# Kernel optimization log

Measured on AMD Instinct MI355X. Metric: run time of the kernel, lower is better.

Reference implementation:

```python
import jax, jax.numpy as jnp
import numpy as np
import math

B, LA, LB, D, H = 8, 2048, 2048, 512, 512

def setup_inputs() -> dict:
    key = jax.random.key(0)
    ks = jax.random.split(key, 6)
    return {
        "input_a": jax.random.normal(ks[0], (B, LA, D), dtype=jnp.float32),
        "input_b": jax.random.normal(ks[1], (B, LB, D), dtype=jnp.float32),
        "mask_a": jax.random.randint(ks[2], (B, LA), 0, 2, dtype=jnp.int32),
        "mask_b": jax.random.randint(ks[3], (B, LB), 0, 2, dtype=jnp.int32),
        "Wa": jax.random.normal(ks[4], (D, H), dtype=jnp.float32) * (1.0 / math.sqrt(D)),
        "ba": jnp.zeros((H,), dtype=jnp.float32),
        "Wb": jax.random.normal(ks[5], (D, H), dtype=jnp.float32) * (1.0 / math.sqrt(D)),
        "bb": jnp.zeros((H,), dtype=jnp.float32),
    }

def reference(input_a, input_b, mask_a, mask_b, Wa, ba, Wb, bb):
    scale = 1.0 / math.sqrt(D)  # math.sqrt(input_dim_a)
    mapped_a = input_a @ Wa + ba            # [B, La, H]
    mapped_b = input_b @ Wb + bb            # [B, Lb, H]
    # final_mask = (mask_a outer mask_b) == 0
    final_mask = (mask_a[:, :, None] * mask_b[:, None, :]) == 0  # [B, La, Lb]
    scores = jnp.einsum('bih,bjh->bij', mapped_a, mapped_b) * scale
    scores = jnp.where(final_mask, jnp.float32(-1e9), scores)
    # attentions_a = softmax over Lb; attentions_b^T = softmax over La axis
    att_a = jax.nn.softmax(scores, axis=-1)   # [B, La, Lb]
    att_bT = jax.nn.softmax(scores, axis=1)   # [B, La, Lb] (= attentions_b.transpose(1,2))
    output_a = jnp.einsum('bij,bjd->bid', att_bT, input_b)  # [B, La, D]
    output_b = jnp.einsum('bij,bid->bjd', att_a, input_a)   # [B, Lb, D]
    return (output_a + input_a, output_b + input_b)
```

## Files before the change

### kernel.cpp

```cpp
#include <hip/hip_runtime.h>
#include <hip/hip_bf16.h>

#define BATCH 8
#define LSEQ 2048
#define DDIM 512

using f32x4 = __attribute__((ext_vector_type(4))) float;
using s16x8 = __attribute__((ext_vector_type(8))) short;

static __device__ __forceinline__ unsigned short f2b(float f) {
  __hip_bfloat16 h = __float2bfloat16(f);
  return __builtin_bit_cast(unsigned short, h);
}
static __device__ __forceinline__ float b2f(unsigned short u) {
  unsigned int v = ((unsigned int)u) << 16;
  return __builtin_bit_cast(float, v);
}

static __device__ __forceinline__ void gld16(const unsigned short* g, unsigned short* l) {
  __builtin_amdgcn_global_load_lds(
      (__attribute__((address_space(1))) void*)(g),
      (__attribute__((address_space(3))) void*)(l), 16, 0, 0);
}

__device__ __forceinline__ void mfma_kloop2(
    const unsigned short* __restrict__ A, const unsigned short* __restrict__ Bt,
    int K, int lda, int ldb, unsigned short* sA, unsigned short* sB,
    int tid, f32x4 acc[4][4]) {
  const int wave = tid >> 6, lane = tid & 63;
  const int wm = (wave >> 1) * 64, wn = (wave & 1) * 64;
  const int lr = lane & 15, lq = lane >> 4;
  const int srow = tid >> 2;
  const int sk = (tid & 3) * 8;
  unsigned short* dA0 = sA + wave * 512;
  unsigned short* dA1 = sA + 2048 + wave * 512;
  unsigned short* dB0 = sB + wave * 512;
  unsigned short* dB1 = sB + 2048 + wave * 512;
  const unsigned short* pa0 = A + (size_t)srow * lda + sk;
  const unsigned short* pa1 = A + (size_t)(srow + 64) * lda + sk;
  const unsigned short* pb0 = Bt + (size_t)srow * ldb + sk;
  const unsigned short* pb1 = Bt + (size_t)(srow + 64) * ldb + sk;
  gld16(pa0, dA0);
  gld16(pa1, dA1);
  gld16(pb0, dB0);
  gld16(pb1, dB1);
  asm volatile("s_waitcnt vmcnt(0)" ::: "memory");
  __builtin_amdgcn_s_barrier();
  int cur = 0;
  for (int k0 = 0; k0 < K; k0 += 32) {
    const int nxt = cur ^ 1;
    if (k0 + 32 < K) {
      const int off = nxt * 4096;
      gld16(pa0 + k0 + 32, dA0 + off);
      gld16(pa1 + k0 + 32, dA1 + off);
      gld16(pb0 + k0 + 32, dB0 + off);
      gld16(pb1 + k0 + 32, dB1 + off);
    }
    const unsigned short* cA = sA + cur * 4096;
    const unsigned short* cB = sB + cur * 4096;
    s16x8 af[4], bf[4];
#pragma unroll
    for (int r = 0; r < 4; ++r)
      af[r] = *(const s16x8*)(cA + (wm + r * 16 + lr) * 32 + lq * 8);
#pragma unroll
    for (int c = 0; c < 4; ++c)
      bf[c] = *(const s16x8*)(cB + (wn + c * 16 + lr) * 32 + lq * 8);
#pragma unroll
    for (int r = 0; r < 4; ++r)
#pragma unroll
      for (int c = 0; c < 4; ++c)
        acc[r][c] = __builtin_amdgcn_mfma_f32_16x16x32_bf16(af[r], bf[c], acc[r][c], 0, 0, 0);
    asm volatile("s_waitcnt vmcnt(0)" ::: "memory");
    __builtin_amdgcn_s_barrier();
    cur = nxt;
  }
}

__global__ __launch_bounds__(256) void k_prep(const float* __restrict__ in_a,
                                              const float* __restrict__ in_b,
                                              const int* __restrict__ ma,
                                              const int* __restrict__ mb,
                                              unsigned short* __restrict__ oa,
                                              unsigned short* __restrict__ ob,
                                              float* __restrict__ Pa,
                                              float* __restrict__ Pb) {
  int z = blockIdx.z;
  const float* in = z ? in_b : in_a;
  const int* mask = z ? mb : ma;
  unsigned short* o16 = z ? ob : oa;
  float* partial = z ? Pb : Pa;
  int b = blockIdx.y;
  int l0 = blockIdx.x * 32;
  __shared__ int sm[32];
  if (threadIdx.x < 32) sm[threadIdx.x] = mask[b * LSEQ + l0 + threadIdx.x];
  __syncthreads();
  int d = threadIdx.x * 2;
  const float* base = in + ((size_t)b * LSEQ + l0) * DDIM + d;
  unsigned short* obase = o16 + ((size_t)b * LSEQ + l0) * DDIM + d;
  float ax = 0.f, ay = 0.f;
#pragma unroll 4
  for (int r = 0; r < 32; ++r) {
    float2 v = *(const float2*)(base + (size_t)r * DDIM);
    ushort2 u; u.x = f2b(v.x); u.y = f2b(v.y);
    *(ushort2*)(obase + (size_t)r * DDIM) = u;
    if (sm[r] == 0) { ax += v.x; ay += v.y; }
  }
  float2 o; o.x = ax; o.y = ay;
  *(float2*)(partial + ((size_t)(b * 64 + blockIdx.x)) * DDIM + d) = o;
}

__global__ __launch_bounds__(256) void k_p2(const float* __restrict__ Pa,
                                            const float* __restrict__ Pb,
                                            float* __restrict__ Ca,
                                            float* __restrict__ Cb) {
  int g = blockIdx.x;
  const float* src = (g < 8) ? Pa : Pb;
  float* dst = (g < 8) ? Ca : Cb;
  int b = g & 7;
  int d = threadIdx.x * 2;
  float ax = 0.f, ay = 0.f;
  for (int c = 0; c < 64; ++c) {
    float2 v = *(const float2*)(src + ((size_t)(b * 64 + c)) * DDIM + d);
    ax += v.x; ay += v.y;
  }
  dst[b * DDIM + d] = ax * (1.0f / LSEQ);
  dst[b * DDIM + d + 1] = ay * (1.0f / LSEQ);
}

__global__ __launch_bounds__(256) void k_transposeW(const float* __restrict__ Wa,
                                                    const float* __restrict__ Wb,
                                                    unsigned short* __restrict__ WaT,
                                                    unsigned short* __restrict__ WbT) {
  int gidx = blockIdx.x * 256 + threadIdx.x;
  const float* W = (gidx < 512 * 512) ? Wa : Wb;
  unsigned short* WT = (gidx < 512 * 512) ? WaT : WbT;
  int idx = gidx & (512 * 512 - 1);
  int h = idx >> 9, d = idx & 511;
  WT[idx] = f2b(W[d * DDIM + h]);
}

__global__ __launch_bounds__(256) void k_gemm_bias(const unsigned short* __restrict__ a16,
                                                   const unsigned short* __restrict__ b16,
                                                   const unsigned short* __restrict__ WaT,
                                                   const unsigned short* __restrict__ WbT,
                                                   const float* __restrict__ ba,
                                                   const float* __restrict__ bb,
                                                   unsigned short* __restrict__ mapa,
                                                   unsigned short* __restrict__ mapb) {
  int id = blockIdx.x;
  int g = id >> 5, rem = id & 31;
  int bn = (rem >> 3) * 128;
  int f = g * 8 + (rem & 7);
  int bm = (f & 127) * 128;
  int z = f >> 7;
  const unsigned short* A = z ? b16 : a16;
  const unsigned short* Bt = z ? WbT : WaT;
  const float* bias = z ? bb : ba;
  unsigned short* Cout = z ? mapb : mapa;
  __shared__ __align__(16) unsigned short sA[2 * 128 * 32], sB[2 * 128 * 32];
  f32x4 acc[4][4];
  f32x4 zero = {0.f, 0.f, 0.f, 0.f};
#pragma unroll
  for (int r = 0; r < 4; ++r)
#pragma unroll
    for (int c = 0; c < 4; ++c) acc[r][c] = zero;
  mfma_kloop2(A + (size_t)bm * DDIM, Bt + (size_t)bn * DDIM, DDIM, DDIM, DDIM,
              sA, sB, threadIdx.x, acc);
  int wave = threadIdx.x >> 6, lane = threadIdx.x & 63;
  int wm = (wave >> 1) * 64, wn = (wave & 1) * 64, lr = lane & 15, lq = lane >> 4;
#pragma unroll
  for (int r = 0; r < 4; ++r)
#pragma unroll
    for (int c = 0; c < 4; ++c)
#pragma unroll
      for (int rr = 0; rr < 4; ++rr) {
        int row = bm + wm + r * 16 + lq * 4 + rr;
        int col = bn + wn + c * 16 + lr;
        Cout[(size_t)row * DDIM + col] = f2b(acc[r][c][rr] + bias[col]);
      }
}

__global__ __launch_bounds__(256) void k_scores(const unsigned short* __restrict__ mapa,
                                                const unsigned short* __restrict__ mapb,
                                                const int* __restrict__ mask_a,
                                                const int* __restrict__ mask_b,
                                                unsigned short* __restrict__ E,
                                                float* __restrict__ Zrow,
                                                float* __restrict__ Zcol) {
  int id = blockIdx.x;
  int low = id & 7, rest = id >> 3;
  int sub = rest & 15, Ghi = rest >> 4;
  int G = Ghi * 8 + low;
  int b = G >> 4, super = G & 15;
  int bi = (((super >> 2) << 2) + (sub >> 2)) * 128;
  int bj = (((super & 3) << 2) + (sub & 3)) * 128;
  __shared__ __align__(16) unsigned short sA[2 * 128 * 32], sB[2 * 128 * 32];
  __shared__ int sMa[128], sMb[128];
  int tid = threadIdx.x;
  if (tid < 128)
    sMa[tid] = mask_a[b * LSEQ + bi + tid];
  else
    sMb[tid - 128] = mask_b[b * LSEQ + bj + tid - 128];
  __syncthreads();
  f32x4 acc[4][4];
  f32x4 zero = {0.f, 0.f, 0.f, 0.f};
#pragma unroll
  for (int r = 0; r < 4; ++r)
#pragma unroll
    for (int c = 0; c < 4; ++c) acc[r][c] = zero;
  mfma_kloop2(mapa + ((size_t)b * LSEQ + bi) * DDIM, mapb + ((size_t)b * LSEQ + bj) * DDIM,
              DDIM, DDIM, DDIM, sA, sB, tid, acc);
  const float scale = 0.044194173824159216f;
  int wave = tid >> 6, lane = tid & 63;
  int wm = (wave >> 1) * 64, wn = (wave & 1) * 64, lr = lane & 15, lq = lane >> 4;
  unsigned short* Eb = E + (size_t)b * LSEQ * LSEQ + (size_t)bi * LSEQ + bj;
  float colp[4] = {0.f, 0.f, 0.f, 0.f};
  float rowp[4][4];
#pragma unroll
  for (int r = 0; r < 4; ++r) {
#pragma unroll
    for (int rr = 0; rr < 4; ++rr) rowp[r][rr] = 0.f;
#pragma unroll
    for (int c = 0; c < 4; ++c) {
      int jl = wn + c * 16 + lr;
      int mb_ = sMb[jl];
#pragma unroll
      for (int rr = 0; rr < 4; ++rr) {
        int il = wm + r * 16 + lq * 4 + rr;
        float e = (sMa[il] && mb_) ? __expf(acc[r][c][rr] * scale) : 0.f;
        rowp[r][rr] += e;
        colp[c] += e;
        Eb[(size_t)il * LSEQ + jl] = f2b(e);
      }
    }
  }
#pragma unroll
  for (int r = 0; r < 4; ++r)
#pragma unroll
    for (int rr = 0; rr < 4; ++rr) {
      float v = rowp[r][rr];
      v += __shfl_xor(v, 1);
      v += __shfl_xor(v, 2);
      v += __shfl_xor(v, 4);
      v += __shfl_xor(v, 8);
      if (lr == 0) {
        int il = wm + r * 16 + lq * 4 + rr;
        atomicAdd(&Zrow[b * LSEQ + bi + il], v);
      }
    }
#pragma unroll
  for (int c = 0; c < 4; ++c) {
    float v = colp[c];
    v += __shfl_xor(v, 16);
    v += __shfl_xor(v, 32);
    if (lq == 0) atomicAdd(&Zcol[b * LSEQ + bj + wn + c * 16 + lr], v);
  }
}

__global__ __launch_bounds__(256) void k_scaleT(const unsigned short* __restrict__ a16,
                                                const unsigned short* __restrict__ b16,
                                                const float* __restrict__ Zrow,
                                                const float* __restrict__ Zcol,
                                                unsigned short* __restrict__ atS,
                                                unsigned short* __restrict__ btS) {
  int zz = blockIdx.z;
  int b = zz & 7, sel = zz >> 3;
  const unsigned short* in = sel ? b16 : a16;
  const float* Z = sel ? Zcol : Zrow;
  unsigned short* out = sel ? btS : atS;
  int i0 = blockIdx.y * 64, d0 = blockIdx.x * 64;
  __shared__ unsigned short lt[64 * 65];
  __shared__ float zinv[64];
  if (threadIdx.x < 64) {
    float z = Z[b * LSEQ + i0 + threadIdx.x];
    zinv[threadIdx.x] = (z > 0.f) ? 1.f / z : 0.f;
  }
  __syncthreads();
  const unsigned short* ib = in + ((size_t)b * LSEQ + i0) * DDIM + d0;
#pragma unroll
  for (int p = 0; p < 16; ++p) {
    int idx = p * 256 + threadIdx.x;
    int dl = idx & 63, il = idx >> 6;
    lt[dl * 65 + il] = f2b(b2f(ib[(size_t)il * DDIM + dl]) * zinv[il]);
  }
  __syncthreads();
  unsigned short* ob = out + ((size_t)b * DDIM + d0) * LSEQ + i0;
#pragma unroll
  for (int p = 0; p < 16; ++p) {
    int idx = p * 256 + threadIdx.x;
    int il = idx & 63, dl = idx >> 6;
    ob[(size_t)dl * LSEQ + il] = lt[dl * 65 + il];
  }
}

__global__ __launch_bounds__(256) void k_gemm_outs(const unsigned short* __restrict__ E,
                                                   const unsigned short* __restrict__ btS,
                                                   const unsigned short* __restrict__ atS,
                                                   const unsigned short* __restrict__ a16,
                                                   const unsigned short* __restrict__ b16,
                                                   const float* __restrict__ Ca,
                                                   const float* __restrict__ Cb,
                                                   float* __restrict__ OutA,
                                                   float* __restrict__ OutB) {
  int id0 = blockIdx.x;
  int modeT = id0 >> 9;
  int id = id0 & 511;
  int g = id >> 5, rem = id & 31;
  int bn = (rem >> 3) * 128;
  int f = g * 8 + (rem & 7);
  int bm = (f & 15) * 128;
  int b = f >> 4;
  const unsigned short* Sop = modeT ? atS : btS;
  const unsigned short* addin = modeT ? b16 : a16;
  const float* Cvec = modeT ? Ca : Cb;
  float* Out = modeT ? OutB : OutA;

  __shared__ __align__(16) unsigned short sA[2 * 128 * 32], sB[2 * 128 * 32];
  int tid = threadIdx.x;
  const int wave = tid >> 6, lane = tid & 63;
  const int wm = (wave >> 1) * 64, wn = (wave & 1) * 64;
  const int lr = lane & 15, lq = lane >> 4;
  f32x4 acc[4][4];
  f32x4 zero = {0.f, 0.f, 0.f, 0.f};
#pragma unroll
  for (int r = 0; r < 4; ++r)
#pragma unroll
    for (int c = 0; c < 4; ++c) acc[r][c] = zero;

  if (!modeT) {
    mfma_kloop2(E + (size_t)b * LSEQ * LSEQ + (size_t)bm * LSEQ,
                Sop + (size_t)b * DDIM * LSEQ + (size_t)bn * LSEQ,
                LSEQ, LSEQ, LSEQ, sA, sB, tid, acc);
  } else {
    const int srow = tid >> 2, sk = (tid & 3) * 8;
    unsigned short* dB0 = sB + wave * 512;
    unsigned short* dB1 = sB + 2048 + wave * 512;
    const unsigned short* Bb = Sop + (size_t)b * DDIM * LSEQ + (size_t)bn * LSEQ;
    const unsigned short* pb0 = Bb + (size_t)srow * LSEQ + sk;
    const unsigned short* pb1 = Bb + (size_t)(srow + 64) * LSEQ + sk;
    const int tc = tid & 15;
    const int tk = tc * 2;
    const int tm = (tid >> 4) * 8;
    const int gq = tc >> 2, wq = tc & 3;
    const unsigned short* pe = E + (size_t)b * LSEQ * LSEQ + (size_t)tk * LSEQ + bm + tm;

    {
      uint4 e0 = *(const uint4*)(pe);
      uint4 e1 = *(const uint4*)(pe + LSEQ);
      gld16(pb0, dB0);
      gld16(pb1, dB1);
      unsigned short t0[8], t1[8];
      *(uint4*)t0 = e0; *(uint4*)t1 = e1;
#pragma unroll
      for (int j = 0; j < 8; ++j) {
        int row = tm + j;
        int sw = gq ^ ((row >> 3) & 3);
        unsigned int v = (unsigned int)t0[j] | ((unsigned int)t1[j] << 16);
        *(unsigned int*)(sA + row * 32 + sw * 8 + wq * 2) = v;
      }
    }
    asm volatile("s_waitcnt vmcnt(0) lgkmcnt(0)" ::: "memory");
    __builtin_amdgcn_s_barrier();
    int cur = 0;
    for (int k0 = 0; k0 < LSEQ; k0 += 32) {
      const int nxt = cur ^ 1;
      const bool more = (k0 + 32 < LSEQ);
      uint4 e0n = {0, 0, 0, 0}, e1n = {0, 0, 0, 0};
      if (more) {
        e0n = *(const uint4*)(pe + (size_t)(k0 + 32) * LSEQ);
        e1n = *(const uint4*)(pe + (size_t)(k0 + 32) * LSEQ + LSEQ);
        gld16(pb0 + k0 + 32, dB0 + nxt * 4096);
        gld16(pb1 + k0 + 32, dB1 + nxt * 4096);
      }
      const unsigned short* cA = sA + cur * 4096;
      const unsigned short* cB = sB + cur * 4096;
      s16x8 af[4], bf[4];
#pragma unroll
      for (int r = 0; r < 4; ++r) {
        int R = wm + r * 16 + lr;
        af[r] = *(const s16x8*)(cA + R * 32 + ((lq ^ ((R >> 3) & 3)) * 8));
      }
#pragma unroll
      for (int c = 0; c < 4; ++c)
        bf[c] = *(const s16x8*)(cB + (wn + c * 16 + lr) * 32 + lq * 8);
#pragma unroll
      for (int r = 0; r < 4; ++r)
#pragma unroll
        for (int c = 0; c < 4; ++c)
          acc[r][c] = __builtin_amdgcn_mfma_f32_16x16x32_bf16(af[r], bf[c], acc[r][c], 0, 0, 0);
      if (more) {
        unsigned short t0[8], t1[8];
        *(uint4*)t0 = e0n; *(uint4*)t1 = e1n;
        unsigned short* nA = sA + nxt * 4096;
#pragma unroll
        for (int j = 0; j < 8; ++j) {
          int row = tm + j;
          int sw = gq ^ ((row >> 3) & 3);
          unsigned int v = (unsigned int)t0[j] | ((unsigned int)t1[j] << 16);
          *(unsigned int*)(nA + row * 32 + sw * 8 + wq * 2) = v;
        }
      }
      asm volatile("s_waitcnt vmcnt(0) lgkmcnt(0)" ::: "memory");
      __builtin_amdgcn_s_barrier();
      cur = nxt;
    }
  }

#pragma unroll
  for (int r = 0; r < 4; ++r)
#pragma unroll
    for (int c = 0; c < 4; ++c)
#pragma unroll
      for (int rr = 0; rr < 4; ++rr) {
        int row = bm + wm + r * 16 + lq * 4 + rr;
        int col = bn + wn + c * 16 + lr;
        size_t o = ((size_t)b * LSEQ + row) * DDIM + col;
        Out[o] = acc[r][c][rr] + b2f(addin[o]) + Cvec[b * DDIM + col];
      }
}

extern "C" void kernel_launch(void* const* d_in, const int* in_sizes, int n_in,
                              void* d_out, int out_size, void* d_ws, size_t ws_size,
                              hipStream_t stream) {
  (void)in_sizes; (void)n_in; (void)out_size; (void)ws_size;
  const float* in_a = (const float*)d_in[0];
  const float* in_b = (const float*)d_in[1];
  const int* ma = (const int*)d_in[2];
  const int* mb = (const int*)d_in[3];
  const float* Wa = (const float*)d_in[4];
  const float* ba = (const float*)d_in[5];
  const float* Wb = (const float*)d_in[6];
  const float* bb = (const float*)d_in[7];
  float* out = (float*)d_out;

  char* ws = (char*)d_ws;
  const size_t MB = 1ull << 20;
  unsigned short* a16 = (unsigned short*)(ws + 0 * MB);
  unsigned short* b16 = (unsigned short*)(ws + 16 * MB);
  unsigned short* WaT = (unsigned short*)(ws + 32 * MB);
  unsigned short* WbT = (unsigned short*)(ws + 32 * MB + 512 * 1024);
  unsigned short* mapa = (unsigned short*)(ws + 33 * MB);
  unsigned short* mapb = (unsigned short*)(ws + 49 * MB);
  unsigned short* E = (unsigned short*)(ws + 65 * MB);
  unsigned short* atS = (unsigned short*)(ws + 129 * MB);
  unsigned short* btS = (unsigned short*)(ws + 145 * MB);
  float* Zrow = (float*)(ws + 161 * MB);
  float* Zcol = (float*)(ws + 161 * MB + 65536);
  float* Ca = (float*)(ws + 161 * MB + 2 * 65536);
  float* Cb = (float*)(ws + 161 * MB + 2 * 65536 + 16384);
  float* Pa = (float*)(ws + 162 * MB);
  float* Pb = (float*)(ws + 163 * MB);

  hipMemsetAsync(Zrow, 0, 2 * 65536, stream);
  k_prep<<<dim3(64, 8, 2), 256, 0, stream>>>(in_a, in_b, ma, mb, a16, b16, Pa, Pb);
  k_transposeW<<<2048, 256, 0, stream>>>(Wa, Wb, WaT, WbT);
  k_p2<<<16, 256, 0, stream>>>(Pa, Pb, Ca, Cb);
  k_gemm_bias<<<1024, 256, 0, stream>>>(a16, b16, WaT, WbT, ba, bb, mapa, mapb);
  k_scores<<<2048, 256, 0, stream>>>(mapa, mapb, ma, mb, E, Zrow, Zcol);
  k_scaleT<<<dim3(8, 32, 16), 256, 0, stream>>>(a16, b16, Zrow, Zcol, atS, btS);
  k_gemm_outs<<<1024, 256, 0, stream>>>(E, btS, atS, a16, b16, Ca, Cb,
                                        out, out + (size_t)BATCH * LSEQ * DDIM);
}
```

Before: 375.6 us.

## Write transposed E in scores kernel and retile output GEMM to 256x256 blocks

Result: no change. 380.5 us (+1.3%).

```diff
diff --git a/kernel.cpp b/kernel.cpp
--- a/kernel.cpp
+++ b/kernel.cpp
@@ -7,6 +7,7 @@
 
 using f32x4 = __attribute__((ext_vector_type(4))) float;
 using s16x8 = __attribute__((ext_vector_type(8))) short;
+using s16x4 = __attribute__((ext_vector_type(4))) short;
 
 static __device__ __forceinline__ unsigned short f2b(float f) {
   __hip_bfloat16 h = __float2bfloat16(f);
@@ -44,8 +45,7 @@
   gld16(pa1, dA1);
   gld16(pb0, dB0);
   gld16(pb1, dB1);
-  asm volatile("s_waitcnt vmcnt(0)" ::: "memory");
-  __builtin_amdgcn_s_barrier();
+  asm volatile("s_waitcnt vmcnt(0)\ns_barrier" ::: "memory");
   int cur = 0;
   for (int k0 = 0; k0 < K; k0 += 32) {
     const int nxt = cur ^ 1;
@@ -70,8 +70,7 @@
 #pragma unroll
       for (int c = 0; c < 4; ++c)
         acc[r][c] = __builtin_amdgcn_mfma_f32_16x16x32_bf16(af[r], bf[c], acc[r][c], 0, 0, 0);
-    asm volatile("s_waitcnt vmcnt(0)" ::: "memory");
-    __builtin_amdgcn_s_barrier();
+    asm volatile("s_waitcnt vmcnt(0)\ns_barrier" ::: "memory");
     cur = nxt;
   }
 }
@@ -185,6 +184,7 @@
                                                 const int* __restrict__ mask_a,
                                                 const int* __restrict__ mask_b,
                                                 unsigned short* __restrict__ E,
+                                                unsigned short* __restrict__ Et,
                                                 float* __restrict__ Zrow,
                                                 float* __restrict__ Zcol) {
   int id = blockIdx.x;
@@ -216,6 +216,7 @@
   unsigned short* Eb = E + (size_t)b * LSEQ * LSEQ + (size_t)bi * LSEQ + bj;
   float colp[4] = {0.f, 0.f, 0.f, 0.f};
   float rowp[4][4];
+  s16x4 ev4[4][4];
 #pragma unroll
   for (int r = 0; r < 4; ++r) {
 #pragma unroll
@@ -230,7 +231,9 @@
         float e = (sMa[il] && mb_) ? __expf(acc[r][c][rr] * scale) : 0.f;
         rowp[r][rr] += e;
         colp[c] += e;
-        Eb[(size_t)il * LSEQ + jl] = f2b(e);
+        unsigned short eb = f2b(e);
+        ev4[r][c][rr] = (short)eb;
+        Eb[(size_t)il * LSEQ + jl] = eb;
       }
     }
   }
@@ -254,6 +257,30 @@
     v += __shfl_xor(v, 16);
     v += __shfl_xor(v, 32);
     if (lq == 0) atomicAdd(&Zcol[b * LSEQ + bj + wn + c * 16 + lr], v);
+  }
+  unsigned short* buf = sA;
+  unsigned short* EtB = Et + (size_t)b * LSEQ * LSEQ + (size_t)bj * LSEQ + bi;
+#pragma unroll
+  for (int half = 0; half < 2; ++half) {
+    __syncthreads();
+    if ((wn != 0) == (half != 0)) {
+#pragma unroll
+      for (int r = 0; r < 4; ++r)
+#pragma unroll
+        for (int c = 0; c < 4; ++c) {
+          int jl = c * 16 + lr;
+          int il0 = wm + r * 16 + lq * 4;
+          *(s16x4*)(buf + jl * 128 + (il0 ^ ((jl & 7) << 4))) = ev4[r][c];
+        }
+    }
+    __syncthreads();
+#pragma unroll
+    for (int p = 0; p < 4; ++p) {
+      int idx = p * 256 + tid;
+      int jlr = idx >> 4, chk = idx & 15;
+      s16x8 v = *(const s16x8*)(buf + jlr * 128 + ((chk * 8) ^ ((jlr & 7) << 4)));
+      *(s16x8*)(EtB + (size_t)(half * 64 + jlr) * LSEQ + chk * 8) = v;
+    }
   }
 }
 
@@ -293,129 +320,109 @@
   }
 }
 
-__global__ __launch_bounds__(256) void k_gemm_outs(const unsigned short* __restrict__ E,
-                                                   const unsigned short* __restrict__ btS,
-                                                   const unsigned short* __restrict__ atS,
-                                                   const unsigned short* __restrict__ a16,
-                                                   const unsigned short* __restrict__ b16,
-                                                   const float* __restrict__ Ca,
-                                                   const float* __restrict__ Cb,
-                                                   float* __restrict__ OutA,
-                                                   float* __restrict__ OutB) {
-  int id0 = blockIdx.x;
-  int modeT = id0 >> 9;
-  int id = id0 & 511;
-  int g = id >> 5, rem = id & 31;
-  int bn = (rem >> 3) * 128;
-  int f = g * 8 + (rem & 7);
-  int bm = (f & 15) * 128;
-  int b = f >> 4;
-  const unsigned short* Sop = modeT ? atS : btS;
-  const unsigned short* addin = modeT ? b16 : a16;
-  const float* Cvec = modeT ? Ca : Cb;
-  float* Out = modeT ? OutB : OutA;
-
-  __shared__ __align__(16) unsigned short sA[2 * 128 * 32], sB[2 * 128 * 32];
-  int tid = threadIdx.x;
+__global__ __launch_bounds__(512, 2) void k_gemm_outs(
+    const unsigned short* __restrict__ E, const unsigned short* __restrict__ Et,
+    const unsigned short* __restrict__ btS, const unsigned short* __restrict__ atS,
+    const unsigned short* __restrict__ a16, const unsigned short* __restrict__ b16,
+    const float* __restrict__ Ca, const float* __restrict__ Cb,
+    float* __restrict__ OutA, float* __restrict__ OutB) {
+  int w = (blockIdx.x & 7) * 32 + (blockIdx.x >> 3);
+  int mode = w >> 7;
+  int r0 = w & 127;
+  int b = r0 >> 4, tile = r0 & 15;
+  int bm = (tile >> 1) * 256, bn = (tile & 1) * 256;
+  const unsigned short* Aop = (mode ? Et : E) + (size_t)b * LSEQ * LSEQ + (size_t)bm * LSEQ;
+  const unsigned short* Bop = (mode ? atS : btS) + (size_t)b * DDIM * LSEQ + (size_t)bn * LSEQ;
+  const unsigned short* addin = mode ? b16 : a16;
+  const float* Cvec = mode ? Ca : Cb;
+  float* Out = mode ? OutB : OutA;
+
+  __shared__ __align__(16) unsigned short sA[4 * 8192], sB[4 * 8192];
+  const int tid = threadIdx.x;
   const int wave = tid >> 6, lane = tid & 63;
-  const int wm = (wave >> 1) * 64, wn = (wave & 1) * 64;
+  const int wr = wave >> 2, wc = wave & 3;
   const int lr = lane & 15, lq = lane >> 4;
-  f32x4 acc[4][4];
+
+  const int srow = tid >> 2;
+  const int kcsw = ((tid & 3) ^ (srow & 3)) * 8;
+  const unsigned short* pa0 = Aop + (size_t)srow * LSEQ + kcsw;
+  const unsigned short* pa1 = pa0 + (size_t)128 * LSEQ;
+  const unsigned short* pb0 = Bop + (size_t)srow * LSEQ + kcsw;
+  const unsigned short* pb1 = pb0 + (size_t)128 * LSEQ;
+  unsigned short* dA = sA + wave * 512;
+  unsigned short* dB = sB + wave * 512;
+
+  int aoff[8], boff[4];
+#pragma unroll
+  for (int m = 0; m < 8; ++m)
+    aoff[m] = (wr * 128 + m * 16 + lr) * 32 + (lq ^ (lr & 3)) * 8;
+#pragma unroll
+  for (int n = 0; n < 4; ++n)
+    boff[n] = (wc * 64 + n * 16 + lr) * 32 + (lq ^ (lr & 3)) * 8;
+
+  f32x4 acc[8][4];
   f32x4 zero = {0.f, 0.f, 0.f, 0.f};
 #pragma unroll
-  for (int r = 0; r < 4; ++r)
-#pragma unroll
-    for (int c = 0; c < 4; ++c) acc[r][c] = zero;
-
-  if (!modeT) {
-    mfma_kloop2(E + (size_t)b * LSEQ * LSEQ + (size_t)bm * LSEQ,
-                Sop + (size_t)b * DDIM * LSEQ + (size_t)bn * LSEQ,
-                LSEQ, LSEQ, LSEQ, sA, sB, tid, acc);
-  } else {
-    const int srow = tid >> 2, sk = (tid & 3) * 8;
-    unsigned short* dB0 = sB + wave * 512;
-    unsigned short* dB1 = sB + 2048 + wave * 512;
-    const unsigned short* Bb = Sop + (size_t)b * DDIM * LSEQ + (size_t)bn * LSEQ;
-    const unsigned short* pb0 = Bb + (size_t)srow * LSEQ + sk;
-    const unsigned short* pb1 = Bb + (size_t)(srow + 64) * LSEQ + sk;
-    const int tc = tid & 15;
-    const int tk = tc * 2;
-    const int tm = (tid >> 4) * 8;
-    const int gq = tc >> 2, wq = tc & 3;
-    const unsigned short* pe = E + (size_t)b * LSEQ * LSEQ + (size_t)tk * LSEQ + bm + tm;
-
-    {
-      uint4 e0 = *(const uint4*)(pe);
-      uint4 e1 = *(const uint4*)(pe + LSEQ);
-      gld16(pb0, dB0);
-      gld16(pb1, dB1);
-      unsigned short t0[8], t1[8];
-      *(uint4*)t0 = e0; *(uint4*)t1 = e1;
-#pragma unroll
-      for (int j = 0; j < 8; ++j) {
-        int row = tm + j;
-        int sw = gq ^ ((row >> 3) & 3);
-        unsigned int v = (unsigned int)t0[j] | ((unsigned int)t1[j] << 16);
-        *(unsigned int*)(sA + row * 32 + sw * 8 + wq * 2) = v;
-      }
-    }
-    asm volatile("s_waitcnt vmcnt(0) lgkmcnt(0)" ::: "memory");
-    __builtin_amdgcn_s_barrier();
-    int cur = 0;
-    for (int k0 = 0; k0 < LSEQ; k0 += 32) {
-      const int nxt = cur ^ 1;
-      const bool more = (k0 + 32 < LSEQ);
-      uint4 e0n = {0, 0, 0, 0}, e1n = {0, 0, 0, 0};
-      if (more) {
-        e0n = *(const uint4*)(pe + (size_t)(k0 + 32) * LSEQ);
-        e1n = *(const uint4*)(pe + (size_t)(k0 + 32) * LSEQ + LSEQ);
-        gld16(pb0 + k0 + 32, dB0 + nxt * 4096);
-        gld16(pb1 + k0 + 32, dB1 + nxt * 4096);
-      }
-      const unsigned short* cA = sA + cur * 4096;
-      const unsigned short* cB = sB + cur * 4096;
-      s16x8 af[4], bf[4];
-#pragma unroll
-      for (int r = 0; r < 4; ++r) {
-        int R = wm + r * 16 + lr;
-        af[r] = *(const s16x8*)(cA + R * 32 + ((lq ^ ((R >> 3) & 3)) * 8));
-      }
-#pragma unroll
-      for (int c = 0; c < 4; ++c)
-        bf[c] = *(const s16x8*)(cB + (wn + c * 16 + lr) * 32 + lq * 8);
-#pragma unroll
-      for (int r = 0; r < 4; ++r)
-#pragma unroll
-        for (int c = 0; c < 4; ++c)
-          acc[r][c] = __builtin_amdgcn_mfma_f32_16x16x32_bf16(af[r], bf[c], acc[r][c], 0, 0, 0);
-      if (more) {
-        unsigned short t0[8], t1[8];
-        *(uint4*)t0 = e0n; *(uint4*)t1 = e1n;
-        unsigned short* nA = sA + nxt * 4096;
-#pragma unroll
-        for (int j = 0; j < 8; ++j) {
-          int row = tm + j;
-          int sw = gq ^ ((row >> 3) & 3);
-          unsigned int v = (unsigned int)t0[j] | ((unsigned int)t1[j] << 16);
-          *(unsigned int*)(nA + row * 32 + sw * 8 + wq * 2) = v;
-        }
-      }
-      asm volatile("s_waitcnt vmcnt(0) lgkmcnt(0)" ::: "memory");
-      __builtin_amdgcn_s_barrier();
-      cur = nxt;
-    }
-  }
-
-#pragma unroll
-  for (int r = 0; r < 4; ++r)
-#pragma unroll
-    for (int c = 0; c < 4; ++c)
+  for (int m = 0; m < 8; ++m)
+#pragma unroll
+    for (int n = 0; n < 4; ++n) acc[m][n] = zero;
+
+#define SGA(c) { const int sl_ = ((c) & 3) * 8192; \
+  gld16(pa0 + (size_t)(c) * 32, dA + sl_); \
+  gld16(pa1 + (size_t)(c) * 32, dA + sl_ + 4096); }
+#define SGB(c) { const int sl_ = ((c) & 3) * 8192; \
+  gld16(pb0 + (size_t)(c) * 32, dB + sl_); \
+  gld16(pb1 + (size_t)(c) * 32, dB + sl_ + 4096); }
+
+  SGA(0); SGB(0); SGA(1); SGB(1); SGA(2); SGB(2);
+  asm volatile("s_waitcnt vmcnt(8)\ns_barrier" ::: "memory");
+
+  for (int j = 0; j < 64; ++j) {
+    const int sl = (j & 3) * 8192;
+    s16x8 af[8];
+#pragma unroll
+    for (int m = 0; m < 8; ++m) af[m] = *(const s16x8*)(sA + sl + aoff[m]);
+    s16x8 bf0 = *(const s16x8*)(sB + sl + boff[0]);
+    s16x8 bf1 = *(const s16x8*)(sB + sl + boff[1]);
+    if (j < 61) SGA(j + 3);
+    __builtin_amdgcn_s_setprio(1);
+#pragma unroll
+    for (int m = 0; m < 8; ++m) {
+      acc[m][0] = __builtin_amdgcn_mfma_f32_16x16x32_bf16(af[m], bf0, acc[m][0], 0, 0, 0);
+      acc[m][1] = __builtin_amdgcn_mfma_f32_16x16x32_bf16(af[m], bf1, acc[m][1], 0, 0, 0);
+    }
+    __builtin_amdgcn_s_setprio(0);
+    asm volatile("s_barrier" ::: "memory");
+    s16x8 bf2 = *(const s16x8*)(sB + sl + boff[2]);
+    s16x8 bf3 = *(const s16x8*)(sB + sl + boff[3]);
+    if (j < 61) SGB(j + 3);
+    __builtin_amdgcn_s_setprio(1);
+#pragma unroll
+    for (int m = 0; m < 8; ++m) {
+      acc[m][2] = __builtin_amdgcn_mfma_f32_16x16x32_bf16(af[m], bf2, acc[m][2], 0, 0, 0);
+      acc[m][3] = __builtin_amdgcn_mfma_f32_16x16x32_bf16(af[m], bf3, acc[m][3], 0, 0, 0);
+    }
+    __builtin_amdgcn_s_setprio(0);
+    if (j < 61)
+      asm volatile("s_waitcnt vmcnt(8)\ns_barrier" ::: "memory");
+    else if (j == 61)
+      asm volatile("s_waitcnt vmcnt(4)\ns_barrier" ::: "memory");
+    else
+      asm volatile("s_waitcnt vmcnt(0)\ns_barrier" ::: "memory");
+  }
+#undef SGA
+#undef SGB
+
+#pragma unroll
+  for (int m = 0; m < 8; ++m)
+#pragma unroll
+    for (int n = 0; n < 4; ++n)
 #pragma unroll
       for (int rr = 0; rr < 4; ++rr) {
-        int row = bm + wm + r * 16 + lq * 4 + rr;
-        int col = bn + wn + c * 16 + lr;
+        int row = bm + wr * 128 + m * 16 + lq * 4 + rr;
+        int col = bn + wc * 64 + n * 16 + lr;
         size_t o = ((size_t)b * LSEQ + row) * DDIM + col;
-        Out[o] = acc[r][c][rr] + b2f(addin[o]) + Cvec[b * DDIM + col];
+        Out[o] = acc[m][n][rr] + b2f(addin[o]) + Cvec[b * DDIM + col];
       }
 }
 
@@ -450,14 +457,15 @@
   float* Cb = (float*)(ws + 161 * MB + 2 * 65536 + 16384);
   float* Pa = (float*)(ws + 162 * MB);
   float* Pb = (float*)(ws + 163 * MB);
+  unsigned short* Et = (unsigned short*)(ws + 164 * MB);
 
   hipMemsetAsync(Zrow, 0, 2 * 65536, stream);
   k_prep<<<dim3(64, 8, 2), 256, 0, stream>>>(in_a, in_b, ma, mb, a16, b16, Pa, Pb);
   k_transposeW<<<2048, 256, 0, stream>>>(Wa, Wb, WaT, WbT);
   k_p2<<<16, 256, 0, stream>>>(Pa, Pb, Ca, Cb);
   k_gemm_bias<<<1024, 256, 0, stream>>>(a16, b16, WaT, WbT, ba, bb, mapa, mapb);
-  k_scores<<<2048, 256, 0, stream>>>(mapa, mapb, ma, mb, E, Zrow, Zcol);
+  k_scores<<<2048, 256, 0, stream>>>(mapa, mapb, ma, mb, E, Et, Zrow, Zcol);
   k_scaleT<<<dim3(8, 32, 16), 256, 0, stream>>>(a16, b16, Zrow, Zcol, atS, btS);
-  k_gemm_outs<<<1024, 256, 0, stream>>>(E, btS, atS, a16, b16, Ca, Cb,
-                                        out, out + (size_t)BATCH * LSEQ * DDIM);
-}
+  k_gemm_outs<<<256, 512, 0, stream>>>(E, Et, btS, atS, a16, b16, Ca, Cb,
+                                       out, out + (size_t)BATCH * LSEQ * DDIM);
+}
```
